# Kernel optimization log

Measured on AMD Instinct MI355X. Metric: run time of the kernel, lower is better.

Reference implementation:

```python
import jax, jax.numpy as jnp
import numpy as np

N_NODES = 65536
N_EDGES = 524288
N_GRAPHS = 1024
NODES_PER_GRAPH = N_NODES // N_GRAPHS
FD = 78  # num_features_xd


def _lin(key, fan_in, fan_out):
    kw, kb = jax.random.split(key)
    s = 1.0 / np.sqrt(fan_in)
    return (jax.random.uniform(kw, (fan_in, fan_out), jnp.float32, -s, s),
            jax.random.uniform(kb, (fan_out,), jnp.float32, -s, s))


def setup_inputs() -> dict:
    key = jax.random.key(0)
    ks = jax.random.split(key, 32)
    inp = {}
    inp["x1"] = jax.random.normal(ks[0], (N_NODES, FD), jnp.float32)
    inp["edge_index1"] = jax.random.randint(ks[1], (2, N_EDGES), 0, N_NODES)
    inp["batch1"] = jnp.arange(N_NODES) // NODES_PER_GRAPH
    inp["x2"] = jax.random.normal(ks[2], (N_NODES, FD), jnp.float32)
    inp["edge_index2"] = jax.random.randint(ks[3], (2, N_EDGES), 0, N_NODES)
    inp["batch2"] = jnp.arange(N_NODES) // NODES_PER_GRAPH
    inp["target"] = jax.random.normal(ks[4], (N_GRAPHS, 1000), jnp.float32)
    # GCN + MLP params for both drug streams
    for i, pre in enumerate(["d1", "d2"]):
        base = 5 + i * 5
        inp[f"{pre}_w1"], inp[f"{pre}_b1"] = _lin(ks[base + 0], FD, FD)
        inp[f"{pre}_w2"], inp[f"{pre}_b2"] = _lin(ks[base + 1], FD, FD * 2)
        inp[f"{pre}_w3"], inp[f"{pre}_b3"] = _lin(ks[base + 2], FD * 2, FD * 4)
        inp[f"{pre}_fc1_w"], inp[f"{pre}_fc1_b"] = _lin(ks[base + 3], FD * 4, 1024)
        inp[f"{pre}_fc2_w"], inp[f"{pre}_fc2_b"] = _lin(ks[base + 4], 1024, 64)
    inp["xt_w"], inp["xt_b"] = _lin(ks[15], 1000, 128)
    inp["fc1_w"], inp["fc1_b"] = _lin(ks[16], 256, 128)
    inp["fc2_w"], inp["fc2_b"] = _lin(ks[17], 128, 32)
    inp["out_w"], inp["out_b"] = _lin(ks[18], 32, 1)
    return inp


def _deg_inv_sqrt(dst, n_nodes):
    # degree with self-loops (PyG add_self_loops then symmetric norm)
    deg = jax.ops.segment_sum(jnp.ones(dst.shape[0], jnp.float32), dst,
                              num_segments=n_nodes) + 1.0
    return jax.lax.rsqrt(deg)


def _gcn_conv(x, w, b, src, dst, dinv):
    # h = X W; out_i = sum_j norm_ij h_j (+ self-loop) + b
    h = x @ w
    coef = dinv[src] * dinv[dst]                      # [E]
    msg = h[src] * coef[:, None]                      # [E, F] gather
    agg = jax.ops.segment_sum(msg, dst, num_segments=x.shape[0])
    agg = agg + h * (dinv * dinv)[:, None]            # self-loop term
    return agg + b


def _drug_branch(x, edge_index, batch, w1, b1, w2, b2, w3, b3,
                 fc1_w, fc1_b, fc2_w, fc2_b):
    src, dst = edge_index[0], edge_index[1]
    dinv = _deg_inv_sqrt(dst, x.shape[0])
    x = jax.nn.relu(_gcn_conv(x, w1, b1, src, dst, dinv))
    x = jax.nn.relu(_gcn_conv(x, w2, b2, src, dst, dinv))
    x = jax.nn.relu(_gcn_conv(x, w3, b3, src, dst, dinv))
    x = jax.ops.segment_max(x, batch, num_segments=N_GRAPHS)  # global max pool
    x = jax.nn.relu(x @ fc1_w + fc1_b)
    # dropout = identity (eval mode)
    return x @ fc2_w + fc2_b


def reference(x1, edge_index1, batch1, x2, edge_index2, batch2, target,
              d1_w1, d1_b1, d1_w2, d1_b2, d1_w3, d1_b3,
              d1_fc1_w, d1_fc1_b, d1_fc2_w, d1_fc2_b,
              d2_w1, d2_b1, d2_w2, d2_b2, d2_w3, d2_b3,
              d2_fc1_w, d2_fc1_b, d2_fc2_w, d2_fc2_b,
              xt_w, xt_b, fc1_w, fc1_b, fc2_w, fc2_b, out_w, out_b):
    g1 = _drug_branch(x1, edge_index1, batch1, d1_w1, d1_b1, d1_w2, d1_b2,
                      d1_w3, d1_b3, d1_fc1_w, d1_fc1_b, d1_fc2_w, d1_fc2_b)
    g2 = _drug_branch(x2, edge_index2, batch2, d2_w1, d2_b1, d2_w2, d2_b2,
                      d2_w3, d2_b3, d2_fc1_w, d2_fc1_b, d2_fc2_w, d2_fc2_b)
    xd = jnp.concatenate([g1, g2], axis=1)            # [G, 128]
    xt = target.reshape(-1, 1000) @ xt_w + xt_b       # [G, 128]
    xc = jnp.concatenate([xd, xt], axis=1)            # [G, 256]
    xc = jax.nn.relu(xc @ fc1_w + fc1_b)
    xc = jax.nn.relu(xc @ fc2_w + fc2_b)
    return xc @ out_w + out_b                         # [G, 1]
```

## Files before the change

kernel.cpp:

```cpp
#include <hip/hip_runtime.h>
#include <hip/hip_bf16.h>
#include <math.h>

#define N_NODES 65536
#define N_EDGES 524288
#define N_GRAPHS 1024
#define NPG 64
#define FD 78
#define RPS 65600
#define BCAP 3072
#define EPB 4096

typedef __attribute__((ext_vector_type(8))) short bf16x8;
typedef __attribute__((ext_vector_type(4))) float f32x4;

__device__ __forceinline__ unsigned short f2bf(float v) {
    unsigned int u = __float_as_uint(v);
    unsigned int r = (u + 0x7FFFu + ((u >> 16) & 1u)) >> 16;
    return (unsigned short)r;
}
__device__ __forceinline__ float bf2f(unsigned short h) {
    return __uint_as_float(((unsigned int)h) << 16);
}

__global__ __launch_bounds__(256, 3) void gemm_mfma(
    const unsigned short* __restrict__ Ah, const unsigned short* __restrict__ Al,
    const unsigned short* __restrict__ Wh, const unsigned short* __restrict__ Wl,
    const float* __restrict__ bias,
    float* __restrict__ Cf, unsigned short* __restrict__ Ch, unsigned short* __restrict__ Cl,
    int N, int Kp, int ldc, int relu, int zpad, int omode)
{
    __shared__ __align__(16) unsigned short sAh[128][40];
    __shared__ __align__(16) unsigned short sAl[128][40];
    __shared__ __align__(16) unsigned short sBh[128][40];
    __shared__ __align__(16) unsigned short sBl[128][40];

    int tid = threadIdx.x;
    int bm = blockIdx.y << 7;
    int bn = blockIdx.x << 7;
    int lane = tid & 63;
    int wid = tid >> 6;
    int wr = wid >> 1, wc = wid & 1;
    int cr = lane & 15;
    int kg = lane >> 4;

    int r0 = tid >> 2;
    int sg = (tid & 3) * 8;
    const unsigned short* pAh = Ah + (size_t)(bm + r0) * Kp + sg;
    const unsigned short* pAl = Al + (size_t)(bm + r0) * Kp + sg;
    const unsigned short* pBh = Wh + (size_t)(bn + r0) * Kp + sg;
    const unsigned short* pBl = Wl + (size_t)(bn + r0) * Kp + sg;
    size_t rstep = (size_t)64 * Kp;

    uint4 vAh0, vAh1, vAl0, vAl1, vBh0, vBh1, vBl0, vBl1;
    auto LOADT = [&](int k0) {
        vAh0 = *(const uint4*)(pAh + k0);
        vAh1 = *(const uint4*)(pAh + k0 + rstep);
        vAl0 = *(const uint4*)(pAl + k0);
        vAl1 = *(const uint4*)(pAl + k0 + rstep);
        vBh0 = *(const uint4*)(pBh + k0);
        vBh1 = *(const uint4*)(pBh + k0 + rstep);
        vBl0 = *(const uint4*)(pBl + k0);
        vBl1 = *(const uint4*)(pBl + k0 + rstep);
    };
    auto WRITET = [&]() {
        *(uint4*)&sAh[r0][sg] = vAh0;
        *(uint4*)&sAh[r0 + 64][sg] = vAh1;
        *(uint4*)&sAl[r0][sg] = vAl0;
        *(uint4*)&sAl[r0 + 64][sg] = vAl1;
        *(uint4*)&sBh[r0][sg] = vBh0;
        *(uint4*)&sBh[r0 + 64][sg] = vBh1;
        *(uint4*)&sBl[r0][sg] = vBl0;
        *(uint4*)&sBl[r0 + 64][sg] = vBl1;
    };

    f32x4 acc[4][4] = {};

    LOADT(0);
    WRITET();
    __syncthreads();

    for (int k0 = 0; k0 < Kp; k0 += 32) {
        int more = (k0 + 32) < Kp;
        if (more) LOADT(k0 + 32);

        bf16x8 bH[4], bL[4];
        #pragma unroll
        for (int nf = 0; nf < 4; ++nf) {
            bH[nf] = *(const bf16x8*)&sBh[wc * 64 + nf * 16 + cr][kg * 8];
            bL[nf] = *(const bf16x8*)&sBl[wc * 64 + nf * 16 + cr][kg * 8];
        }
        #pragma unroll
        for (int mf = 0; mf < 4; ++mf) {
            bf16x8 aH = *(const bf16x8*)&sAh[wr * 64 + mf * 16 + cr][kg * 8];
            bf16x8 aL = *(const bf16x8*)&sAl[wr * 64 + mf * 16 + cr][kg * 8];
            #pragma unroll
            for (int nf = 0; nf < 4; ++nf) {
                acc[mf][nf] = __builtin_amdgcn_mfma_f32_16x16x32_bf16(aH, bH[nf], acc[mf][nf], 0, 0, 0);
                acc[mf][nf] = __builtin_amdgcn_mfma_f32_16x16x32_bf16(aH, bL[nf], acc[mf][nf], 0, 0, 0);
                acc[mf][nf] = __builtin_amdgcn_mfma_f32_16x16x32_bf16(aL, bH[nf], acc[mf][nf], 0, 0, 0);
            }
        }
        __syncthreads();
        if (more) {
            WRITET();
            __syncthreads();
        }
    }

    if (omode == 2) {
        int g = (blockIdx.y << 1) + wr;
        #pragma unroll
        for (int nf = 0; nf < 4; ++nf) {
            int col = bn + wc * 64 + nf * 16 + cr;
            if (col < N) {
                float m = -INFINITY;
                #pragma unroll
                for (int mf = 0; mf < 4; ++mf) {
                    f32x4 v = acc[mf][nf];
                    #pragma unroll
                    for (int j = 0; j < 4; ++j) m = fmaxf(m, v[j]);
                }
                m = fmaxf(m + bias[col], 0.f);
                m = fmaxf(m, __shfl_xor(m, 16, 64));
                m = fmaxf(m, __shfl_xor(m, 32, 64));
                if (kg == 0)
                    atomicMax((unsigned int*)&Cf[(size_t)g * ldc + col], __float_as_uint(m));
            }
        }
        return;
    }

    #pragma unroll
    for (int mf = 0; mf < 4; ++mf) {
        int rowbase = bm + wr * 64 + mf * 16 + kg * 4;
        #pragma unroll
        for (int nf = 0; nf < 4; ++nf) {
            int col = bn + wc * 64 + nf * 16 + cr;
            if (col >= ldc) continue;
            int live = col < N;
            if (!live && !zpad) continue;
            float bv = live ? bias[col] : 0.f;
            f32x4 v = acc[mf][nf];
            #pragma unroll
            for (int j = 0; j < 4; ++j) {
                size_t idx = (size_t)(rowbase + j) * ldc + col;
                float o = v[j] + bv;
                if (relu) o = fmaxf(o, 0.f);
                if (!live) o = 0.f;
                if (omode == 0) {
                    Cf[idx] = o;
                } else {
                    unsigned short h = f2bf(o);
                    Ch[idx] = h;
                    Cl[idx] = f2bf(o - bf2f(h));
                }
            }
        }
    }
}

__global__ __launch_bounds__(256) void gemm_mfma_sk(
    const unsigned short* __restrict__ Ah, const unsigned short* __restrict__ Al,
    const unsigned short* __restrict__ Wh, const unsigned short* __restrict__ Wl,
    const float* __restrict__ bias, float* __restrict__ C,
    int Kp, int ldc, int kchunk)
{
    __shared__ __align__(16) unsigned short sAh[128][40];
    __shared__ __align__(16) unsigned short sAl[128][40];
    __shared__ __align__(16) unsigned short sBh[64][40];
    __shared__ __align__(16) unsigned short sBl[64][40];

    int tid = threadIdx.x;
    int bm = blockIdx.y << 7;
    int bn = blockIdx.x << 6;
    int kbase = blockIdx.z * kchunk;
    int lane = tid & 63;
    int wid = tid >> 6;
    int wr = wid >> 1, wc = wid & 1;
    int cr = lane & 15;
    int kg = lane >> 4;

    f32x4 acc[4][2] = {};

    for (int k0 = kbase; k0 < kbase + kchunk; k0 += 32) {
        #pragma unroll
        for (int s = tid; s < 512; s += 256) {
            int r = s >> 2, seg = s & 3;
            *(uint4*)&sAh[r][seg * 8] =
                *(const uint4*)(Ah + (size_t)(bm + r) * Kp + k0 + seg * 8);
        }
        #pragma unroll
        for (int s = tid; s < 512; s += 256) {
            int r = s >> 2, seg = s & 3;
            *(uint4*)&sAl[r][seg * 8] =
                *(const uint4*)(Al + (size_t)(bm + r) * Kp + k0 + seg * 8);
        }
        {
            int r = tid >> 2, seg = tid & 3;
            *(uint4*)&sBh[r][seg * 8] =
                *(const uint4*)(Wh + (size_t)(bn + r) * Kp + k0 + seg * 8);
            *(uint4*)&sBl[r][seg * 8] =
                *(const uint4*)(Wl + (size_t)(bn + r) * Kp + k0 + seg * 8);
        }
        __syncthreads();

        bf16x8 bH[2], bL[2];
        #pragma unroll
        for (int nf = 0; nf < 2; ++nf) {
            bH[nf] = *(const bf16x8*)&sBh[wc * 32 + nf * 16 + cr][kg * 8];
            bL[nf] = *(const bf16x8*)&sBl[wc * 32 + nf * 16 + cr][kg * 8];
        }
        #pragma unroll
        for (int mf = 0; mf < 4; ++mf) {
            bf16x8 aH = *(const bf16x8*)&sAh[wr * 64 + mf * 16 + cr][kg * 8];
            bf16x8 aL = *(const bf16x8*)&sAl[wr * 64 + mf * 16 + cr][kg * 8];
            #pragma unroll
            for (int nf = 0; nf < 2; ++nf) {
                acc[mf][nf] = __builtin_amdgcn_mfma_f32_16x16x32_bf16(aH, bH[nf], acc[mf][nf], 0, 0, 0);
                acc[mf][nf] = __builtin_amdgcn_mfma_f32_16x16x32_bf16(aH, bL[nf], acc[mf][nf], 0, 0, 0);
                acc[mf][nf] = __builtin_amdgcn_mfma_f32_16x16x32_bf16(aL, bH[nf], acc[mf][nf], 0, 0, 0);
            }
        }
        __syncthreads();
    }

    int z0 = blockIdx.z == 0;
    #pragma unroll
    for (int mf = 0; mf < 4; ++mf) {
        int rowbase = bm + wr * 64 + mf * 16 + kg * 4;
        #pragma unroll
        for (int nf = 0; nf < 2; ++nf) {
            int col = bn + wc * 32 + nf * 16 + cr;
            float bv = z0 ? bias[col] : 0.f;
            f32x4 v = acc[mf][nf];
            #pragma unroll
            for (int j = 0; j < 4; ++j)
                atomicAdd(&C[(size_t)(rowbase + j) * ldc + col], v[j] + bv);
        }
    }
}

struct PrepDesc { const float* W; unsigned short* Wh; unsigned short* Wl; int K, N, Kp, Np; };
struct PrepArgs { PrepDesc d[11]; };

__global__ void prep_all(PrepArgs pa) {
    PrepDesc de = pa.d[blockIdx.y];
    int tot = de.Np * de.Kp;
    for (int t = blockIdx.x * blockDim.x + threadIdx.x; t < tot; t += gridDim.x * blockDim.x) {
        int n = t / de.Kp, k = t - n * de.Kp;
        float v = (n < de.N && k < de.K) ? de.W[(size_t)k * de.N + n] : 0.f;
        unsigned short h = f2bf(v);
        de.Wh[t] = h;
        de.Wl[t] = f2bf(v - bf2f(h));
    }
}

__global__ void split_pad(const float* __restrict__ x, unsigned short* __restrict__ Xh,
                          unsigned short* __restrict__ Xl, int M, int F, int Kp) {
    int t = blockIdx.x * blockDim.x + threadIdx.x;
    if (t >= M * Kp) return;
    int i = t / Kp, c = t - i * Kp;
    float v = (c < F) ? x[(size_t)i * F + c] : 0.f;
    unsigned short h = f2bf(v);
    Xh[t] = h;
    Xl[t] = f2bf(v - bf2f(h));
}

__global__ __launch_bounds__(256) void fc_row(
    const float* __restrict__ A, const float* __restrict__ B,
    const float* __restrict__ bias, float* __restrict__ C,
    int M, int N, int K, int lda, int ldc, int relu)
{
    int nchunks = (N + 63) >> 6;
    int bid = blockIdx.x;
    int nc = bid % nchunks;
    int m = ((bid / nchunks) << 2) + (threadIdx.x >> 6);
    int lane = threadIdx.x & 63;
    if (m >= M) return;
    int n = (nc << 6) + lane;
    int nclamp = n < N ? n : N - 1;
    const float* __restrict__ a = A + (size_t)m * lda;
    const float* __restrict__ bp = B + nclamp;
    float acc = 0.f;
    int kk = 0;
    #pragma unroll 4
    for (; kk + 4 <= K; kk += 4) {
        float a0 = a[kk + 0], a1 = a[kk + 1], a2 = a[kk + 2], a3 = a[kk + 3];
        float b0 = bp[(size_t)(kk + 0) * N];
        float b1 = bp[(size_t)(kk + 1) * N];
        float b2 = bp[(size_t)(kk + 2) * N];
        float b3 = bp[(size_t)(kk + 3) * N];
        acc = fmaf(a0, b0, acc);
        acc = fmaf(a1, b1, acc);
        acc = fmaf(a2, b2, acc);
        acc = fmaf(a3, b3, acc);
    }
    for (; kk < K; ++kk)
        acc = fmaf(a[kk], bp[(size_t)kk * N], acc);
    if (n < N) {
        float v = acc + bias[n];
        if (relu) v = fmaxf(v, 0.f);
        C[(size_t)m * ldc + n] = v;
    }
}

__global__ __launch_bounds__(1024) void bucket_scatter(
    const int* __restrict__ s1, const int* __restrict__ d1,
    const int* __restrict__ s2, const int* __restrict__ d2,
    int* __restrict__ bcnt, unsigned int* __restrict__ bbuf, int E)
{
    __shared__ int lhist[256];
    __shared__ int lbase[256];
    int nblk = E / EPB;
    int b = blockIdx.x >= nblk;
    int blk = blockIdx.x - b * nblk;
    const int* sp = b ? s2 : s1;
    const int* dp = b ? d2 : d1;
    int e0 = blk * EPB;
    if (threadIdx.x < 256) lhist[threadIdx.x] = 0;
    __syncthreads();

    unsigned int pack[EPB / 1024];
    int bkt[EPB / 1024], rank[EPB / 1024];
    #pragma unroll
    for (int i = 0; i < EPB / 1024; ++i) {
        int e = e0 + threadIdx.x + i * 1024;
        int s = sp[e], d = dp[e];
        bkt[i] = d >> 8;
        pack[i] = ((unsigned int)s << 8) | (unsigned int)(d & 255);
        rank[i] = atomicAdd(&lhist[bkt[i]], 1);
    }
    __syncthreads();
    if (threadIdx.x < 256) {
        int c = lhist[threadIdx.x];
        lbase[threadIdx.x] = c ? atomicAdd(&bcnt[(b << 8) | threadIdx.x], c) : 0;
    }
    __syncthreads();
    #pragma unroll
    for (int i = 0; i < EPB / 1024; ++i) {
        int pos = lbase[bkt[i]] + rank[i];
        if (pos < BCAP)
            bbuf[(size_t)((b << 8) | bkt[i]) * BCAP + pos] = pack[i];
    }
}

__global__ __launch_bounds__(256) void bucket_count(const int* __restrict__ bcnt,
                                                    const unsigned int* __restrict__ bbuf,
                                                    int* __restrict__ cntB) {
    __shared__ int lc[256];
    int bk = blockIdx.x;
    lc[threadIdx.x] = 0;
    __syncthreads();
    int n = bcnt[bk]; if (n > BCAP) n = BCAP;
    const unsigned int* p = bbuf + (size_t)bk * BCAP;
    for (int i = threadIdx.x; i < n; i += 256)
        atomicAdd(&lc[p[i] & 255u], 1);
    __syncthreads();
    int br = bk >> 8, nb = (bk & 255) << 8;
    cntB[br * N_NODES + nb + threadIdx.x] = lc[threadIdx.x];
}

__global__ __launch_bounds__(256) void bucket_sort(const int* __restrict__ bcnt,
                                                   const unsigned int* __restrict__ bbuf,
                                                   const int* __restrict__ rowpB,
                                                   int* __restrict__ csrsB) {
    __shared__ int lrow[256];
    __shared__ int lcur[256];
    int bk = blockIdx.x;
    int br = bk >> 8, nb = (bk & 255) << 8;
    lrow[threadIdx.x] = rowpB[br * RPS + nb + threadIdx.x];
    lcur[threadIdx.x] = 0;
    __syncthreads();
    int n = bcnt[bk]; if (n > BCAP) n = BCAP;
    const unsigned int* p = bbuf + (size_t)bk * BCAP;
    int* outp = csrsB + (size_t)br * N_EDGES;
    for (int i = threadIdx.x; i < n; i += 256) {
        unsigned int e = p[i];
        int dl = e & 255u;
        int pos = lrow[dl] + atomicAdd(&lcur[dl], 1);
        outp[pos] = (int)(e >> 8);
    }
}

__global__ void make_dinv2(const int* __restrict__ cnt, float* __restrict__ dinv) {
    int t = blockIdx.x * blockDim.x + threadIdx.x;
    if (t < 2 * N_NODES) dinv[t] = rsqrtf((float)cnt[t] + 1.0f);
}

__global__ __launch_bounds__(1024) void scan_rowptr(const int* __restrict__ cntB,
                                                    int* __restrict__ rowpB) {
    __shared__ int sums[1024];
    const int* cnt = cntB + blockIdx.x * N_NODES;
    int* row_ptr = rowpB + blockIdx.x * RPS;
    int t = threadIdx.x;
    int base = t * 64;
    int s = 0;
    #pragma unroll 4
    for (int i = 0; i < 64; ++i) s += cnt[base + i];
    sums[t] = s;
    __syncthreads();
    for (int off = 1; off < 1024; off <<= 1) {
        int v = sums[t];
        int add = (t >= off) ? sums[t - off] : 0;
        __syncthreads();
        sums[t] = v + add;
        __syncthreads();
    }
    int run = (t == 0) ? 0 : sums[t - 1];
    for (int i = 0; i < 64; ++i) {
        row_ptr[base + i] = run;
        run += cnt[base + i];
    }
    if (t == 1023) row_ptr[N_NODES] = run;
}

__global__ void repack_pad(const float* __restrict__ x, float* __restrict__ xp,
                           int F, int S) {
    int t = blockIdx.x * blockDim.x + threadIdx.x;
    int total = N_NODES * S;
    if (t >= total) return;
    int i = t / S, c = t - i * S;
    xp[t] = (c < F) ? x[(size_t)i * F + c] : 0.f;
}

__global__ __launch_bounds__(256) void gather8(
    const float* __restrict__ x, const int* __restrict__ rowp,
    const int* __restrict__ csrs, const float* __restrict__ dinv,
    unsigned short* __restrict__ Ah, unsigned short* __restrict__ Al,
    int S, int Kp)
{
    int Kp8 = Kp >> 3;
    int t = blockIdx.x * blockDim.x + threadIdx.x;
    int total = N_NODES * Kp8;
    if (t >= total) return;
    int i = t / Kp8;
    int g = t - i * Kp8;
    int f = g << 3;
    size_t ob = (size_t)i * Kp + f;
    if (f >= S) {
        bf16x8 z = {};
        *(bf16x8*)&Ah[ob] = z;
        *(bf16x8*)&Al[ob] = z;
        return;
    }
    float di = dinv[i];
    const float* xr = x + (size_t)i * S + f;
    f32x4 s0 = *(const f32x4*)xr;
    f32x4 s1 = *(const f32x4*)(xr + 4);
    float w = di * di;
    s0 *= w;
    s1 *= w;
    int p0 = rowp[i], p1 = rowp[i + 1];
    int p = p0;
    for (; p + 4 <= p1; p += 4) {
        int sa = csrs[p], sb = csrs[p + 1], sc = csrs[p + 2], sd = csrs[p + 3];
        float ca = dinv[sa] * di, cb = dinv[sb] * di;
        float cc = dinv[sc] * di, cd = dinv[sd] * di;
        const float* ra = x + (size_t)sa * S + f;
        const float* rb = x + (size_t)sb * S + f;
        const float* rc = x + (size_t)sc * S + f;
        const float* rd = x + (size_t)sd * S + f;
        f32x4 a0 = *(const f32x4*)ra, a1 = *(const f32x4*)(ra + 4);
        f32x4 b0 = *(const f32x4*)rb, b1 = *(const f32x4*)(rb + 4);
        f32x4 c0 = *(const f32x4*)rc, c1 = *(const f32x4*)(rc + 4);
        f32x4 d0 = *(const f32x4*)rd, d1 = *(const f32x4*)(rd + 4);
        s0 += ca * a0 + cb * b0 + cc * c0 + cd * d0;
        s1 += ca * a1 + cb * b1 + cc * c1 + cd * d1;
    }
    for (; p < p1; ++p) {
        int sa = csrs[p];
        float ca = dinv[sa] * di;
        const float* ra = x + (size_t)sa * S + f;
        s0 += ca * *(const f32x4*)ra;
        s1 += ca * *(const f32x4*)(ra + 4);
    }
    bf16x8 hh, ll;
    #pragma unroll
    for (int j = 0; j < 4; ++j) {
        unsigned short h0 = f2bf(s0[j]);
        hh[j] = (short)h0;
        ll[j] = (short)f2bf(s0[j] - bf2f(h0));
        unsigned short h1 = f2bf(s1[j]);
        hh[4 + j] = (short)h1;
        ll[4 + j] = (short)f2bf(s1[j] - bf2f(h1));
    }
    *(bf16x8*)&Ah[ob] = hh;
    *(bf16x8*)&Al[ob] = ll;
}

static inline void fc_launch(const float* A, const float* B, const float* bias, float* C,
                             int M, int N, int K, int lda, int ldc, int relu, hipStream_t s) {
    int nchunks = (N + 63) / 64;
    int mblocks = (M + 3) / 4;
    fc_row<<<nchunks * mblocks, 256, 0, s>>>(A, B, bias, C, M, N, K, lda, ldc, relu);
}

extern "C" void kernel_launch(void* const* d_in, const int* in_sizes, int n_in,
                              void* d_out, int out_size, void* d_ws, size_t ws_size,
                              hipStream_t stream) {
    (void)in_sizes; (void)n_in; (void)out_size; (void)ws_size;

    const float* x1     = (const float*)d_in[0];
    const int*   ei1    = (const int*)d_in[1];
    const float* x2     = (const float*)d_in[3];
    const int*   ei2    = (const int*)d_in[4];
    const float* target = (const float*)d_in[6];

    const float* xt_w  = (const float*)d_in[27];
    const float* xt_b  = (const float*)d_in[28];
    const float* fc1_w = (const float*)d_in[29];
    const float* fc1_b = (const float*)d_in[30];
    const float* fc2_w = (const float*)d_in[31];
    const float* fc2_b = (const float*)d_in[32];
    const float* out_w = (const float*)d_in[33];
    const float* out_b = (const float*)d_in[34];

    char* ws = (char*)d_ws;
    unsigned short* Ahb = (unsigned short*)(ws + 0);
    unsigned short* Alb = (unsigned short*)(ws + 20971520);
    float* Y3   = (float*)(ws + 41943040);
    char*  S2   = ws + 123731968;
    int*   csrsB = (int*) (ws + 165675008);
    int*   rowpB = (int*) (ws + 169869312);
    int*   cntB  = (int*) (ws + 170394112);
    float* dinvB = (float*)(ws + 170918400);
    float* xc   = (float*)(ws + 171442688);
    float* xc1  = (float*)(ws + 172491264);
    float* xc2  = (float*)(ws + 173015552);
    unsigned short* wt    = (unsigned short*)(ws + 173146624);
    unsigned short* wtfc1 = (unsigned short*)(ws + 173933056);
    unsigned short* wtfc2 = (unsigned short*)(ws + 176554496);
    unsigned short* wtxt  = (unsigned short*)(ws + 177603072);

    unsigned int* bbuf = (unsigned int*)Ahb;
    int*          bcnt = (int*)Alb;

    float* xpad = Y3;
    float* y1   = Y3;
    float* y2   = (float*)S2;
    unsigned short* Ph = (unsigned short*)(S2 + 0);
    unsigned short* Pl = (unsigned short*)(S2 + 655360);
    unsigned short* Fh = (unsigned short*)(S2 + 1310720);
    unsigned short* Fl = (unsigned short*)(S2 + 3407872);
    unsigned short* Th = (unsigned short*)(S2 + 5505024);
    unsigned short* Tl = (unsigned short*)(S2 + 7602176);
    float* pooled = (float*)(S2 + 9699328);

    const int E = N_EDGES;

    const int Ks[3]  = { FD, FD, FD * 2 };
    const int Ns[3]  = { FD, FD * 2, FD * 4 };
    const int Kps[3] = { 96, 96, 160 };
    const int Nps[3] = { 128, 256, 384 };
    const int Ss[3]  = { 80, 80, 160 };
    const int Ldc[3] = { 80, 160, 312 };
    const int wtoff[3] = { 0, 24576, 73728 };
    const int WT_BRANCH = 196608;

    PrepArgs pa;
    for (int br = 0; br < 2; ++br) {
        int base = 7 + br * 10;
        for (int c = 0; c < 3; ++c) {
            unsigned short* wh = wt + br * WT_BRANCH + wtoff[c];
            pa.d[br * 3 + c] = { (const float*)d_in[base + 2 * c], wh,
                                 wh + Nps[c] * Kps[c], Ks[c], Ns[c], Kps[c], Nps[c] };
        }
        pa.d[6 + br] = { (const float*)d_in[base + 6], wtfc1 + br * 655360,
                         wtfc1 + br * 655360 + 327680, FD * 4, 1024, 320, 1024 };
        pa.d[8 + br] = { (const float*)d_in[base + 8], wtfc2 + br * 262144,
                         wtfc2 + br * 262144 + 131072, 1024, 64, 1024, 128 };
    }
    pa.d[10] = { xt_w, wtxt, wtxt + 131072, 1000, 128, 1024, 128 };
    prep_all<<<dim3(256, 11), 256, 0, stream>>>(pa);

    const int* src1 = ei1, *dst1 = ei1 + E;
    const int* src2 = ei2, *dst2 = ei2 + E;
    hipMemsetAsync(bcnt, 0, 512 * sizeof(int), stream);
    bucket_scatter<<<2 * (E / EPB), 1024, 0, stream>>>(src1, dst1, src2, dst2, bcnt, bbuf, E);
    bucket_count<<<512, 256, 0, stream>>>(bcnt, bbuf, cntB);
    make_dinv2<<<(2 * N_NODES + 255) / 256, 256, 0, stream>>>(cntB, dinvB);
    scan_rowptr<<<2, 1024, 0, stream>>>(cntB, rowpB);
    bucket_sort<<<512, 256, 0, stream>>>(bcnt, bbuf, rowpB, csrsB);

    hipMemsetAsync(xc, 0, N_GRAPHS * 256 * sizeof(float), stream);

    for (int br = 0; br < 2; ++br) {
        const float* x = br == 0 ? x1 : x2;
        const int* rowp = rowpB + br * RPS;
        const int* csr  = csrsB + br * E;
        const float* dv = dinvB + br * N_NODES;
        int base = 7 + br * 10;
        const float* bias_c[3] = { (const float*)d_in[base + 1], (const float*)d_in[base + 3],
                                   (const float*)d_in[base + 5] };
        const float* bfc1b = (const float*)d_in[base + 7];
        const float* bfc2b = (const float*)d_in[base + 9];

        repack_pad<<<(N_NODES * 80 + 255) / 256, 256, 0, stream>>>(x, xpad, FD, 80);

        const float* cin[3]  = { xpad, y1, y2 };
        float*       cout[3] = { y1, y2, pooled };
        for (int c = 0; c < 3; ++c) {
            int Kp = Kps[c], Np = Nps[c], S = Ss[c];
            int total = N_NODES * (Kp >> 3);
            gather8<<<(total + 255) / 256, 256, 0, stream>>>(
                cin[c], rowp, csr, dv, Ahb, Alb, S, Kp);
            if (c == 2) {
                hipMemsetAsync(pooled, 0, N_GRAPHS * 320 * sizeof(float), stream);
                gemm_mfma<<<dim3(Np / 128, 512), 256, 0, stream>>>(
                    Ahb, Alb, wt + br * WT_BRANCH + wtoff[c],
                    wt + br * WT_BRANCH + wtoff[c] + Np * Kp, bias_c[c],
                    pooled, nullptr, nullptr, Ns[c], Kp, 320, 1, 0, 2);
            } else {
                gemm_mfma<<<dim3(Np / 128, 512), 256, 0, stream>>>(
                    Ahb, Alb, wt + br * WT_BRANCH + wtoff[c],
                    wt + br * WT_BRANCH + wtoff[c] + Np * Kp, bias_c[c],
                    cout[c], nullptr, nullptr, Ns[c], Kp, Ldc[c], 1, 1, 0);
            }
        }

        split_pad<<<(N_GRAPHS * 320 + 255) / 256, 256, 0, stream>>>(pooled, Ph, Pl, N_GRAPHS, 320, 320);
        gemm_mfma<<<dim3(8, 8), 256, 0, stream>>>(
            Ph, Pl, wtfc1 + br * 655360, wtfc1 + br * 655360 + 327680, bfc1b,
            nullptr, Fh, Fl, 1024, 320, 1024, 1, 1, 1);
        gemm_mfma_sk<<<dim3(1, 8, 8), 256, 0, stream>>>(
            Fh, Fl, wtfc2 + br * 262144, wtfc2 + br * 262144 + 131072, bfc2b,
            xc + br * 64, 1024, 256, 128);
    }

    split_pad<<<(1024 * 1024 + 255) / 256, 256, 0, stream>>>(target, Th, Tl, 1024, 1000, 1024);
    gemm_mfma_sk<<<dim3(2, 8, 8), 256, 0, stream>>>(
        Th, Tl, wtxt, wtxt + 131072, xt_b,
        xc + 128, 1024, 256, 128);

    fc_launch(xc,  fc1_w, fc1_b, xc1, N_GRAPHS, 128, 256, 256, 128, 1, stream);
    fc_launch(xc1, fc2_w, fc2_b, xc2, N_GRAPHS, 32, 128, 128, 32, 1, stream);
    fc_launch(xc2, out_w, out_b, (float*)d_out, N_GRAPHS, 1, 32, 32, 1, 0, stream);
}
```

Baseline: 586.0 us.

## Batch both drug branches into single launches per GCN layer and MLP stage

```diff
diff --git a/kernel.cpp b/kernel.cpp
--- a/kernel.cpp
+++ b/kernel.cpp
@@ -25,10 +25,11 @@
 
 __global__ __launch_bounds__(256, 3) void gemm_mfma(
     const unsigned short* __restrict__ Ah, const unsigned short* __restrict__ Al,
-    const unsigned short* __restrict__ Wh, const unsigned short* __restrict__ Wl,
-    const float* __restrict__ bias,
+    const unsigned short* __restrict__ Wh0, const unsigned short* __restrict__ Wl0,
+    const unsigned short* __restrict__ Wh1, const unsigned short* __restrict__ Wl1,
+    const float* __restrict__ bias0, const float* __restrict__ bias1,
     float* __restrict__ Cf, unsigned short* __restrict__ Ch, unsigned short* __restrict__ Cl,
-    int N, int Kp, int ldc, int relu, int zpad, int omode)
+    int N, int Kp, int ldc, int relu, int zpad, int omode, int brshift)
 {
     __shared__ __align__(16) unsigned short sAh[128][40];
     __shared__ __align__(16) unsigned short sAl[128][40];
@@ -38,6 +39,11 @@
     int tid = threadIdx.x;
     int bm = blockIdx.y << 7;
     int bn = blockIdx.x << 7;
+    int b = blockIdx.y >> brshift;
+    const unsigned short* Wh = b ? Wh1 : Wh0;
+    const unsigned short* Wl = b ? Wl1 : Wl0;
+    const float* bias = b ? bias1 : bias0;
+
     int lane = tid & 63;
     int wid = tid >> 6;
     int wr = wid >> 1, wc = wid & 1;
@@ -162,9 +168,10 @@
 
 __global__ __launch_bounds__(256) void gemm_mfma_sk(
     const unsigned short* __restrict__ Ah, const unsigned short* __restrict__ Al,
-    const unsigned short* __restrict__ Wh, const unsigned short* __restrict__ Wl,
-    const float* __restrict__ bias, float* __restrict__ C,
-    int Kp, int ldc, int kchunk)
+    const unsigned short* __restrict__ Wh0, const unsigned short* __restrict__ Wl0,
+    const unsigned short* __restrict__ Wh1, const unsigned short* __restrict__ Wl1,
+    const float* __restrict__ bias0, const float* __restrict__ bias1,
+    float* __restrict__ C, int Kp, int ldc, int kchunk, int brshift, int colstep)
 {
     __shared__ __align__(16) unsigned short sAh[128][40];
     __shared__ __align__(16) unsigned short sAl[128][40];
@@ -174,6 +181,11 @@
     int tid = threadIdx.x;
     int bm = blockIdx.y << 7;
     int bn = blockIdx.x << 6;
+    int b = blockIdx.y >> brshift;
+    const unsigned short* Wh = b ? Wh1 : Wh0;
+    const unsigned short* Wl = b ? Wl1 : Wl0;
+    const float* bias = b ? bias1 : bias0;
+    int rowoff = bm - (b << 10);
     int kbase = blockIdx.z * kchunk;
     int lane = tid & 63;
     int wid = tid >> 6;
@@ -228,11 +240,12 @@
     int z0 = blockIdx.z == 0;
     #pragma unroll
     for (int mf = 0; mf < 4; ++mf) {
-        int rowbase = bm + wr * 64 + mf * 16 + kg * 4;
+        int rowbase = rowoff + wr * 64 + mf * 16 + kg * 4;
         #pragma unroll
         for (int nf = 0; nf < 2; ++nf) {
-            int col = bn + wc * 32 + nf * 16 + cr;
-            float bv = z0 ? bias[col] : 0.f;
+            int cl = bn + wc * 32 + nf * 16 + cr;
+            float bv = z0 ? bias[cl] : 0.f;
+            int col = b * colstep + cl;
             f32x4 v = acc[mf][nf];
             #pragma unroll
             for (int j = 0; j < 4; ++j)
@@ -415,24 +428,26 @@
     if (t == 1023) row_ptr[N_NODES] = run;
 }
 
-__global__ void repack_pad(const float* __restrict__ x, float* __restrict__ xp,
-                           int F, int S) {
+__global__ void repack_pad2(const float* __restrict__ x1, const float* __restrict__ x2,
+                            float* __restrict__ xp) {
     int t = blockIdx.x * blockDim.x + threadIdx.x;
-    int total = N_NODES * S;
+    int total = 2 * N_NODES * 80;
     if (t >= total) return;
-    int i = t / S, c = t - i * S;
-    xp[t] = (c < F) ? x[(size_t)i * F + c] : 0.f;
+    int i = t / 80, c = t - i * 80;
+    int b = i >> 16, il = i & 65535;
+    const float* x = b ? x2 : x1;
+    xp[t] = (c < FD) ? x[(size_t)il * FD + c] : 0.f;
 }
 
 __global__ __launch_bounds__(256) void gather8(
-    const float* __restrict__ x, const int* __restrict__ rowp,
-    const int* __restrict__ csrs, const float* __restrict__ dinv,
+    const float* __restrict__ x, const int* __restrict__ rowpB,
+    const int* __restrict__ csrsB, const float* __restrict__ dinvB,
     unsigned short* __restrict__ Ah, unsigned short* __restrict__ Al,
     int S, int Kp)
 {
     int Kp8 = Kp >> 3;
     int t = blockIdx.x * blockDim.x + threadIdx.x;
-    int total = N_NODES * Kp8;
+    int total = 2 * N_NODES * Kp8;
     if (t >= total) return;
     int i = t / Kp8;
     int g = t - i * Kp8;
@@ -444,23 +459,28 @@
         *(bf16x8*)&Al[ob] = z;
         return;
     }
-    float di = dinv[i];
+    int b = i >> 16, il = i & 65535;
+    const int* rowp = rowpB + b * RPS;
+    const int* csrs = csrsB + (size_t)b * N_EDGES;
+    const float* dinv = dinvB + ((size_t)b << 16);
+    const float* xb = x + (((size_t)b << 16) * S);
+    float di = dinv[il];
     const float* xr = x + (size_t)i * S + f;
     f32x4 s0 = *(const f32x4*)xr;
     f32x4 s1 = *(const f32x4*)(xr + 4);
     float w = di * di;
     s0 *= w;
     s1 *= w;
-    int p0 = rowp[i], p1 = rowp[i + 1];
+    int p0 = rowp[il], p1 = rowp[il + 1];
     int p = p0;
     for (; p + 4 <= p1; p += 4) {
         int sa = csrs[p], sb = csrs[p + 1], sc = csrs[p + 2], sd = csrs[p + 3];
         float ca = dinv[sa] * di, cb = dinv[sb] * di;
         float cc = dinv[sc] * di, cd = dinv[sd] * di;
-        const float* ra = x + (size_t)sa * S + f;
-        const float* rb = x + (size_t)sb * S + f;
-        const float* rc = x + (size_t)sc * S + f;
-        const float* rd = x + (size_t)sd * S + f;
+        const float* ra = xb + (size_t)sa * S + f;
+        const float* rb = xb + (size_t)sb * S + f;
+        const float* rc = xb + (size_t)sc * S + f;
+        const float* rd = xb + (size_t)sd * S + f;
         f32x4 a0 = *(const f32x4*)ra, a1 = *(const f32x4*)(ra + 4);
         f32x4 b0 = *(const f32x4*)rb, b1 = *(const f32x4*)(rb + 4);
         f32x4 c0 = *(const f32x4*)rc, c1 = *(const f32x4*)(rc + 4);
@@ -471,7 +491,7 @@
     for (; p < p1; ++p) {
         int sa = csrs[p];
         float ca = dinv[sa] * di;
-        const float* ra = x + (size_t)sa * S + f;
+        const float* ra = xb + (size_t)sa * S + f;
         s0 += ca * *(const f32x4*)ra;
         s1 += ca * *(const f32x4*)(ra + 4);
     }
@@ -517,35 +537,36 @@
     const float* out_b = (const float*)d_in[34];
 
     char* ws = (char*)d_ws;
-    unsigned short* Ahb = (unsigned short*)(ws + 0);
-    unsigned short* Alb = (unsigned short*)(ws + 20971520);
-    float* Y3   = (float*)(ws + 41943040);
-    char*  S2   = ws + 123731968;
-    int*   csrsB = (int*) (ws + 165675008);
-    int*   rowpB = (int*) (ws + 169869312);
-    int*   cntB  = (int*) (ws + 170394112);
-    float* dinvB = (float*)(ws + 170918400);
-    float* xc   = (float*)(ws + 171442688);
-    float* xc1  = (float*)(ws + 172491264);
-    float* xc2  = (float*)(ws + 173015552);
-    unsigned short* wt    = (unsigned short*)(ws + 173146624);
-    unsigned short* wtfc1 = (unsigned short*)(ws + 173933056);
-    unsigned short* wtfc2 = (unsigned short*)(ws + 176554496);
-    unsigned short* wtxt  = (unsigned short*)(ws + 177603072);
-
-    unsigned int* bbuf = (unsigned int*)Ahb;
-    int*          bcnt = (int*)Alb;
-
-    float* xpad = Y3;
-    float* y1   = Y3;
-    float* y2   = (float*)S2;
-    unsigned short* Ph = (unsigned short*)(S2 + 0);
-    unsigned short* Pl = (unsigned short*)(S2 + 655360);
-    unsigned short* Fh = (unsigned short*)(S2 + 1310720);
-    unsigned short* Fl = (unsigned short*)(S2 + 3407872);
-    unsigned short* Th = (unsigned short*)(S2 + 5505024);
-    unsigned short* Tl = (unsigned short*)(S2 + 7602176);
-    float* pooled = (float*)(S2 + 9699328);
+    unsigned short* AhB = (unsigned short*)(ws + 0);
+    unsigned short* AlB = (unsigned short*)(ws + 41943040);
+    float* R1   = (float*)(ws + 83886080);
+    float* Y2   = (float*)(ws + 83886080);
+    char*  FCS  = ws + 83886080;
+    int*   csrsB = (int*) (ws + 167772160);
+    int*   rowpB = (int*) (ws + 171966464);
+    int*   cntB  = (int*) (ws + 172491264);
+    float* dinvB = (float*)(ws + 173015552);
+    float* xc   = (float*)(ws + 173539840);
+    float* xc1  = (float*)(ws + 174588416);
+    float* xc2  = (float*)(ws + 175112704);
+    unsigned short* wt    = (unsigned short*)(ws + 175243776);
+    unsigned short* wtfc1 = (unsigned short*)(ws + 176030208);
+    unsigned short* wtfc2 = (unsigned short*)(ws + 178651648);
+    unsigned short* wtxt  = (unsigned short*)(ws + 179700224);
+
+    unsigned int* bbuf = (unsigned int*)AhB;
+    int*          bcnt = (int*)AlB;
+
+    float* xpad = R1;
+    float* y1   = R1;
+    float* y2   = Y2;
+    float*          pooled = (float*)(FCS + 0);
+    unsigned short* Ph = (unsigned short*)(FCS + 2621440);
+    unsigned short* Pl = (unsigned short*)(FCS + 3932160);
+    unsigned short* Fh = (unsigned short*)(FCS + 5242880);
+    unsigned short* Fl = (unsigned short*)(FCS + 9437184);
+    unsigned short* Th = (unsigned short*)(FCS + 13631488);
+    unsigned short* Tl = (unsigned short*)(FCS + 15728640);
 
     const int E = N_EDGES;
 
@@ -554,7 +575,7 @@
     const int Kps[3] = { 96, 96, 160 };
     const int Nps[3] = { 128, 256, 384 };
     const int Ss[3]  = { 80, 80, 160 };
-    const int Ldc[3] = { 80, 160, 312 };
+    const int Ldc[3] = { 80, 160, 320 };
     const int wtoff[3] = { 0, 24576, 73728 };
     const int WT_BRANCH = 196608;
 
@@ -585,53 +606,53 @@
 
     hipMemsetAsync(xc, 0, N_GRAPHS * 256 * sizeof(float), stream);
 
+    repack_pad2<<<(2 * N_NODES * 80 + 255) / 256, 256, 0, stream>>>(x1, x2, xpad);
+
+    const float* cin[3]  = { xpad, y1, y2 };
+    float*       cout[3] = { y1, y2, pooled };
+    const float* biasc[2][3];
     for (int br = 0; br < 2; ++br) {
-        const float* x = br == 0 ? x1 : x2;
-        const int* rowp = rowpB + br * RPS;
-        const int* csr  = csrsB + br * E;
-        const float* dv = dinvB + br * N_NODES;
         int base = 7 + br * 10;
-        const float* bias_c[3] = { (const float*)d_in[base + 1], (const float*)d_in[base + 3],
-                                   (const float*)d_in[base + 5] };
-        const float* bfc1b = (const float*)d_in[base + 7];
-        const float* bfc2b = (const float*)d_in[base + 9];
-
-        repack_pad<<<(N_NODES * 80 + 255) / 256, 256, 0, stream>>>(x, xpad, FD, 80);
-
-        const float* cin[3]  = { xpad, y1, y2 };
-        float*       cout[3] = { y1, y2, pooled };
-        for (int c = 0; c < 3; ++c) {
-            int Kp = Kps[c], Np = Nps[c], S = Ss[c];
-            int total = N_NODES * (Kp >> 3);
-            gather8<<<(total + 255) / 256, 256, 0, stream>>>(
-                cin[c], rowp, csr, dv, Ahb, Alb, S, Kp);
-            if (c == 2) {
-                hipMemsetAsync(pooled, 0, N_GRAPHS * 320 * sizeof(float), stream);
-                gemm_mfma<<<dim3(Np / 128, 512), 256, 0, stream>>>(
-                    Ahb, Alb, wt + br * WT_BRANCH + wtoff[c],
-                    wt + br * WT_BRANCH + wtoff[c] + Np * Kp, bias_c[c],
-                    pooled, nullptr, nullptr, Ns[c], Kp, 320, 1, 0, 2);
-            } else {
-                gemm_mfma<<<dim3(Np / 128, 512), 256, 0, stream>>>(
-                    Ahb, Alb, wt + br * WT_BRANCH + wtoff[c],
-                    wt + br * WT_BRANCH + wtoff[c] + Np * Kp, bias_c[c],
-                    cout[c], nullptr, nullptr, Ns[c], Kp, Ldc[c], 1, 1, 0);
-            }
-        }
-
-        split_pad<<<(N_GRAPHS * 320 + 255) / 256, 256, 0, stream>>>(pooled, Ph, Pl, N_GRAPHS, 320, 320);
-        gemm_mfma<<<dim3(8, 8), 256, 0, stream>>>(
-            Ph, Pl, wtfc1 + br * 655360, wtfc1 + br * 655360 + 327680, bfc1b,
-            nullptr, Fh, Fl, 1024, 320, 1024, 1, 1, 1);
-        gemm_mfma_sk<<<dim3(1, 8, 8), 256, 0, stream>>>(
-            Fh, Fl, wtfc2 + br * 262144, wtfc2 + br * 262144 + 131072, bfc2b,
-            xc + br * 64, 1024, 256, 128);
-    }
+        biasc[br][0] = (const float*)d_in[base + 1];
+        biasc[br][1] = (const float*)d_in[base + 3];
+        biasc[br][2] = (const float*)d_in[base + 5];
+    }
+
+    for (int c = 0; c < 3; ++c) {
+        int Kp = Kps[c], Np = Nps[c], S = Ss[c];
+        int total = 2 * N_NODES * (Kp >> 3);
+        gather8<<<(total + 255) / 256, 256, 0, stream>>>(
+            cin[c], rowpB, csrsB, dinvB, AhB, AlB, S, Kp);
+        unsigned short* wh0 = wt + wtoff[c];
+        unsigned short* wh1 = wt + WT_BRANCH + wtoff[c];
+        if (c == 2) {
+            hipMemsetAsync(pooled, 0, 2048 * 320 * sizeof(float), stream);
+            gemm_mfma<<<dim3(Np / 128, 1024), 256, 0, stream>>>(
+                AhB, AlB, wh0, wh0 + Np * Kp, wh1, wh1 + Np * Kp,
+                biasc[0][2], biasc[1][2],
+                pooled, nullptr, nullptr, Ns[c], Kp, 320, 1, 0, 2, 9);
+        } else {
+            gemm_mfma<<<dim3(Np / 128, 1024), 256, 0, stream>>>(
+                AhB, AlB, wh0, wh0 + Np * Kp, wh1, wh1 + Np * Kp,
+                biasc[0][c], biasc[1][c],
+                cout[c], nullptr, nullptr, Ns[c], Kp, Ldc[c], 1, 1, 0, 9);
+        }
+    }
+
+    split_pad<<<(2048 * 320 + 255) / 256, 256, 0, stream>>>(pooled, Ph, Pl, 2048, 320, 320);
+    gemm_mfma<<<dim3(8, 16), 256, 0, stream>>>(
+        Ph, Pl, wtfc1, wtfc1 + 327680, wtfc1 + 655360, wtfc1 + 655360 + 327680,
+        (const float*)d_in[7 + 7], (const float*)d_in[17 + 7],
+        nullptr, Fh, Fl, 1024, 320, 1024, 1, 1, 1, 3);
+    gemm_mfma_sk<<<dim3(1, 16, 8), 256, 0, stream>>>(
+        Fh, Fl, wtfc2, wtfc2 + 131072, wtfc2 + 262144, wtfc2 + 262144 + 131072,
+        (const float*)d_in[7 + 9], (const float*)d_in[17 + 9],
+        xc, 1024, 256, 128, 3, 64);
 
     split_pad<<<(1024 * 1024 + 255) / 256, 256, 0, stream>>>(target, Th, Tl, 1024, 1000, 1024);
     gemm_mfma_sk<<<dim3(2, 8, 8), 256, 0, stream>>>(
-        Th, Tl, wtxt, wtxt + 131072, xt_b,
-        xc + 128, 1024, 256, 128);
+        Th, Tl, wtxt, wtxt + 131072, wtxt, wtxt + 131072, xt_b, xt_b,
+        xc + 128, 1024, 256, 128, 30, 0);
 
     fc_launch(xc,  fc1_w, fc1_b, xc1, N_GRAPHS, 128, 256, 256, 128, 1, stream);
     fc_launch(xc1, fc2_w, fc2_b, xc2, N_GRAPHS, 32, 128, 128, 32, 1, stream);
```

New measurement: 519.2 us. 1.13x faster.
